# Optimization experiments

Hardware: AMD Instinct MI355X
Metric: run time of the kernel (lower is better)

Reference implementation:

```python
import jax, jax.numpy as jnp
import numpy as np

K = 2  # top-k slots from init kwargs


def setup_inputs() -> dict:
    key = jax.random.key(0)
    ks = jax.random.split(key, 6)
    B, T, d, E, dff = 2, 2048, 512, 8, 2048
    x = jax.random.normal(ks[0], (B, T, d), dtype=jnp.float32)
    Wg = jax.random.normal(ks[1], (d, E), dtype=jnp.float32) * 0.02
    W1 = jax.random.normal(ks[2], (E, d, dff), dtype=jnp.float32) * 0.02
    b1 = jnp.zeros((E, dff), dtype=jnp.float32)
    W2 = jax.random.normal(ks[3], (E, dff, d), dtype=jnp.float32) * 0.02
    b2 = jnp.zeros((E, d), dtype=jnp.float32)
    return {"x": x, "Wg": Wg, "W1": W1, "b1": b1, "W2": W2, "b2": b2}


def reference(x, Wg, W1, b1, W2, b2):
    # Gate: softmax over experts, top-k probs renormalized. Note: in the
    # original code the per-expert gather/scatter masks partition the tokens,
    # so dispatched_input == x * p_i (full weighted input), and ALL experts'
    # MLPs are applied to it and summed (tf.add_n). We reproduce that math.
    logits = jnp.einsum('btd,de->bte', x, Wg)          # [B,T,E]
    probs = jax.nn.softmax(logits, axis=-1)
    top_p, _top_i = jax.lax.top_k(probs, K)            # [B,T,K]
    top_p = top_p / jnp.sum(top_p, axis=-1, keepdims=True)
    b2_sum = jnp.sum(b2, axis=0)                        # sum of all experts' output biases
    out = jnp.zeros_like(x)
    for i in range(K):  # small fixed loop over top-k slots
        w_in = x * top_p[..., i:i + 1]                  # [B,T,d]
        # every expert runs on the full weighted input (faithful to source)
        h = jax.nn.gelu(
            jnp.einsum('btd,edf->ebtf', w_in, W1) + b1[:, None, None, :],
            approximate=False)                           # [E,B,T,dff]
        out = out + jnp.einsum('ebtf,efd->btd', h, W2) + b2_sum
    return out
```

## Files before the change

### kernel.cpp

```cpp
#include <hip/hip_runtime.h>
#include <hip/hip_bf16.h>
#include <cstdint>

#define TOKENS 4096
#define DMODEL 512
#define NEXP 8
#define DFF 2048

typedef short s16x8 __attribute__((ext_vector_type(8)));
typedef short s16x4 __attribute__((ext_vector_type(4)));
typedef float f32x4 __attribute__((ext_vector_type(4)));
typedef unsigned int u32x2 __attribute__((ext_vector_type(2)));

__device__ __forceinline__ float bf2f(short h) {
    unsigned int u = ((unsigned int)(unsigned short)h) << 16;
    return __uint_as_float(u);
}
__device__ __forceinline__ short f2bf(float f) {
    unsigned int u = __float_as_uint(f);
    u += 0x7fffu + ((u >> 16) & 1u);
    return (short)(u >> 16);
}
__device__ __forceinline__ unsigned int cvtpk_bf16(float a, float b) {
    unsigned int r;
    asm volatile("v_cvt_pk_bf16_f32 %0, %1, %2" : "=v"(r) : "v"(a), "v"(b));
    return r;
}
#define GP_C0 2.3022084f
#define GP_C1 0.10294330f
__device__ __forceinline__ float gelu_pair(float x0, float x1) {
    float z0 = x0 * fmaf(x0 * x0, GP_C1, GP_C0);
    float z1 = x1 * fmaf(x1 * x1, GP_C1, GP_C0);
    float e0 = __builtin_amdgcn_exp2f(z0);
    float e1 = __builtin_amdgcn_exp2f(z1);
    float t0 = 1.0f + e0, t1 = 1.0f + e1;
    float R = __builtin_amdgcn_rcpf(t0 * t1);
    float num = fmaf(x0, t1, x1 * t0);
    return fmaf(-num, R, x0 + x1);
}
__device__ __forceinline__ void gload_lds16(const void* g, void* l) {
    __builtin_amdgcn_global_load_lds((const __attribute__((address_space(1))) void*)g,
                                     (__attribute__((address_space(3))) void*)l, 16, 0, 0);
}

__global__ void gate_cvt_kernel(const float* __restrict__ x, const float* __restrict__ Wg,
                                float* __restrict__ s0, float* __restrict__ s1,
                                short* __restrict__ xb) {
    int wave = threadIdx.x >> 6;
    int lane = threadIdx.x & 63;
    int t = blockIdx.x * 4 + wave;
    const float* xr = x + (size_t)t * DMODEL + lane * 8;
    float4 xa = *(const float4*)(xr);
    float4 xv2 = *(const float4*)(xr + 4);
    float xv[8] = {xa.x, xa.y, xa.z, xa.w, xv2.x, xv2.y, xv2.z, xv2.w};
    s16x8 v;
#pragma unroll
    for (int j = 0; j < 8; j++) v[j] = f2bf(xv[j]);
    *(s16x8*)&xb[(size_t)t * DMODEL + lane * 8] = v;

    float lg[8];
#pragma unroll
    for (int e = 0; e < 8; e++) lg[e] = 0.f;
#pragma unroll
    for (int j = 0; j < 8; j++) {
        const float4* wr = (const float4*)(Wg + (size_t)(lane * 8 + j) * NEXP);
        float4 wa = wr[0], wb = wr[1];
        lg[0] = fmaf(xv[j], wa.x, lg[0]);
        lg[1] = fmaf(xv[j], wa.y, lg[1]);
        lg[2] = fmaf(xv[j], wa.z, lg[2]);
        lg[3] = fmaf(xv[j], wa.w, lg[3]);
        lg[4] = fmaf(xv[j], wb.x, lg[4]);
        lg[5] = fmaf(xv[j], wb.y, lg[5]);
        lg[6] = fmaf(xv[j], wb.z, lg[6]);
        lg[7] = fmaf(xv[j], wb.w, lg[7]);
    }
#pragma unroll
    for (int off = 32; off > 0; off >>= 1) {
#pragma unroll
        for (int e = 0; e < 8; e++) lg[e] += __shfl_xor(lg[e], off, 64);
    }
    float l0 = lg[0]; int i0 = 0;
#pragma unroll
    for (int e = 1; e < 8; e++) { if (lg[e] > l0) { l0 = lg[e]; i0 = e; } }
    float l1 = -3.4e38f;
#pragma unroll
    for (int e = 0; e < 8; e++) { if (e != i0 && lg[e] > l1) l1 = lg[e]; }
    float p1 = expf(l1 - l0);
    float sa = 1.0f / (1.0f + p1);
    if (lane == 0) { s0[t] = sa; s1[t] = p1 * sa; }
}

__global__ void transpose_cvt2_kernel(const float* __restrict__ W1, short* __restrict__ w1t,
                                      const float* __restrict__ W2, short* __restrict__ w2t) {
    __shared__ float t[64][33];
    int b = blockIdx.y;
    int bid = blockIdx.x;
    const float* ip;
    short* op;
    int R, C, tx, ty;
    if (bid < 512) {
        R = 512; C = 2048; tx = bid & 31; ty = bid >> 5;
        ip = W1 + (size_t)b * R * C; op = w1t + (size_t)b * R * C;
    } else {
        int id = bid - 512;
        R = 2048; C = 512; tx = id & 7; ty = id >> 3;
        ip = W2 + (size_t)b * R * C; op = w2t + (size_t)b * R * C;
    }
    int c0 = tx * 64, r0 = ty * 32;
    int tid = threadIdx.x;
    int lr = tid >> 3, lc8 = (tid & 7) * 8;
    const float* src = &ip[(size_t)(r0 + lr) * C + c0 + lc8];
    float4 v0 = *(const float4*)src;
    float4 v1 = *(const float4*)(src + 4);
    t[lc8 + 0][lr] = v0.x; t[lc8 + 1][lr] = v0.y; t[lc8 + 2][lr] = v0.z; t[lc8 + 3][lr] = v0.w;
    t[lc8 + 4][lr] = v1.x; t[lc8 + 5][lr] = v1.y; t[lc8 + 6][lr] = v1.z; t[lc8 + 7][lr] = v1.w;
    __syncthreads();
    int sc = tid >> 2, sk = (tid & 3) * 8;
    s16x8 o;
#pragma unroll
    for (int j = 0; j < 8; j++) o[j] = f2bf(t[sc][sk + j]);
    *(s16x8*)&op[(size_t)(c0 + sc) * R + r0 + sk] = o;
}

__launch_bounds__(256, 2)
__global__ void gemm1_kernel(const short* __restrict__ xb, const short* __restrict__ w1t,
                             const float* __restrict__ s0v, const float* __restrict__ s1v,
                             const float* __restrict__ b1, short* __restrict__ H) {
    __shared__ short Al[128 * 64];
    __shared__ short Bl[128 * 64];
    __shared__ float ls0[128], ls1[128], lb1[128];
    int d = blockIdx.x;
    int e = d & 7;
    int tno = d >> 3;
    int n0 = (tno & 15) * 128;
    int m0 = (tno >> 4) * 128;
    const short* A = xb;
    const short* B = w1t + (size_t)e * DFF * DMODEL;
    short* Ho = H + (size_t)e * TOKENS * DFF;

    int tid = threadIdx.x;
    int lane = tid & 63;
    int w = tid >> 6;
    int m_off = (w >> 1) * 64;
    int n_off = (w & 1) * 64;

    if (tid < 128) {
        ls0[tid] = s0v[m0 + tid];
        ls1[tid] = s1v[m0 + tid];
        lb1[tid] = b1[(size_t)e * DFF + n0 + tid];
    }

    int srow = lane >> 3;
    int schunk = (lane & 7) ^ srow;
    int q = lane >> 4;

    f32x4 acc[4][4];
#pragma unroll
    for (int mi = 0; mi < 4; mi++)
#pragma unroll
        for (int ni = 0; ni < 4; ni++) acc[mi][ni] = (f32x4){0.f, 0.f, 0.f, 0.f};

    for (int k0 = 0; k0 < DMODEL; k0 += 64) {
#pragma unroll
        for (int c = 0; c < 4; c++) {
            int seg = c * 4 + w;
            gload_lds16(&A[(size_t)(m0 + seg * 8 + srow) * DMODEL + k0 + schunk * 8],
                        &Al[seg * 512]);
            gload_lds16(&B[(size_t)(n0 + seg * 8 + srow) * DMODEL + k0 + schunk * 8],
                        &Bl[seg * 512]);
        }
        __syncthreads();
#pragma unroll
        for (int ks = 0; ks < 2; ks++) {
            s16x8 af[4], bfr[4];
#pragma unroll
            for (int mi = 0; mi < 4; mi++) {
                int r = m_off + mi * 16 + (lane & 15);
                int cp = (ks * 4 + q) ^ (r & 7);
                af[mi] = *(const s16x8*)&Al[r * 64 + cp * 8];
            }
#pragma unroll
            for (int ni = 0; ni < 4; ni++) {
                int r = n_off + ni * 16 + (lane & 15);
                int cp = (ks * 4 + q) ^ (r & 7);
                bfr[ni] = *(const s16x8*)&Bl[r * 64 + cp * 8];
            }
#pragma unroll
            for (int mi = 0; mi < 4; mi++)
#pragma unroll
                for (int ni = 0; ni < 4; ni++)
                    acc[mi][ni] = __builtin_amdgcn_mfma_f32_16x16x32_bf16(bfr[ni], af[mi], acc[mi][ni], 0, 0, 0);
        }
        __syncthreads();
    }
    {
        int mcol = lane & 15;
        int nrow4 = (lane >> 4) * 4;
#pragma unroll
        for (int mi = 0; mi < 4; mi++) {
            int m = m_off + mi * 16 + mcol;
            float sa = ls0[m], sb = ls1[m];
#pragma unroll
            for (int ni = 0; ni < 4; ni++) {
                int nb = n_off + ni * 16 + nrow4;
                float4 bb = *(const float4*)&lb1[nb];
                float bv[4] = {bb.x, bb.y, bb.z, bb.w};
                float h4[4];
#pragma unroll
                for (int r = 0; r < 4; r++) {
                    float a = acc[mi][ni][r];
                    h4[r] = gelu_pair(fmaf(sa, a, bv[r]), fmaf(sb, a, bv[r]));
                }
                u32x2 pv;
                pv[0] = cvtpk_bf16(h4[0], h4[1]);
                pv[1] = cvtpk_bf16(h4[2], h4[3]);
                *(u32x2*)&Ho[(size_t)(m0 + m) * DFF + n0 + nb] = pv;
            }
        }
    }
}

__launch_bounds__(256, 2)
__global__ void gemm2_kernel(const short* __restrict__ H, const short* __restrict__ w2t,
                             short* __restrict__ partb) {
    __shared__ short Al[128 * 64];
    __shared__ short Bl[128 * 64];
    int d = blockIdx.x;
    int e = d & 7;
    int tno = d >> 3;
    int n0 = (tno & 3) * 128;
    int m0 = (tno >> 2) * 128;
    const short* A = H + (size_t)e * TOKENS * DFF;
    const short* B = w2t + (size_t)e * DMODEL * DFF;
    short* Pe = partb + (size_t)e * TOKENS * DMODEL;

    int tid = threadIdx.x;
    int lane = tid & 63;
    int w = tid >> 6;
    int m_off = (w >> 1) * 64;
    int n_off = (w & 1) * 64;

    int srow = lane >> 3;
    int schunk = (lane & 7) ^ srow;
    int q = lane >> 4;

    f32x4 acc[4][4];
#pragma unroll
    for (int mi = 0; mi < 4; mi++)
#pragma unroll
        for (int ni = 0; ni < 4; ni++) acc[mi][ni] = (f32x4){0.f, 0.f, 0.f, 0.f};

    for (int k0 = 0; k0 < DFF; k0 += 64) {
#pragma unroll
        for (int c = 0; c < 4; c++) {
            int seg = c * 4 + w;
            gload_lds16(&A[(size_t)(m0 + seg * 8 + srow) * DFF + k0 + schunk * 8],
                        &Al[seg * 512]);
            gload_lds16(&B[(size_t)(n0 + seg * 8 + srow) * DFF + k0 + schunk * 8],
                        &Bl[seg * 512]);
        }
        __syncthreads();
#pragma unroll
        for (int ks = 0; ks < 2; ks++) {
            s16x8 af[4], bfr[4];
#pragma unroll
            for (int mi = 0; mi < 4; mi++) {
                int r = m_off + mi * 16 + (lane & 15);
                int cp = (ks * 4 + q) ^ (r & 7);
                af[mi] = *(const s16x8*)&Al[r * 64 + cp * 8];
            }
#pragma unroll
            for (int ni = 0; ni < 4; ni++) {
                int r = n_off + ni * 16 + (lane & 15);
                int cp = (ks * 4 + q) ^ (r & 7);
                bfr[ni] = *(const s16x8*)&Bl[r * 64 + cp * 8];
            }
#pragma unroll
            for (int mi = 0; mi < 4; mi++)
#pragma unroll
                for (int ni = 0; ni < 4; ni++)
                    acc[mi][ni] = __builtin_amdgcn_mfma_f32_16x16x32_bf16(bfr[ni], af[mi], acc[mi][ni], 0, 0, 0);
        }
        __syncthreads();
    }

    {
        int mcol = lane & 15;
        int nrow4 = (lane >> 4) * 4;
#pragma unroll
        for (int mi = 0; mi < 4; mi++) {
            int m = m0 + m_off + mi * 16 + mcol;
#pragma unroll
            for (int ni = 0; ni < 4; ni++) {
                int nb = n0 + n_off + ni * 16 + nrow4;
                u32x2 pv;
                pv[0] = cvtpk_bf16(acc[mi][ni][0], acc[mi][ni][1]);
                pv[1] = cvtpk_bf16(acc[mi][ni][2], acc[mi][ni][3]);
                *(u32x2*)&Pe[(size_t)m * DMODEL + nb] = pv;
            }
        }
    }
}

__global__ void reduce_kernel(const short* __restrict__ partb, const float* __restrict__ b2,
                              float* __restrict__ out) {
    int i = (blockIdx.x * 256 + threadIdx.x) * 8;
    if (i >= TOKENS * DMODEL) return;
    int n = i & (DMODEL - 1);
    float s[8] = {0.f, 0.f, 0.f, 0.f, 0.f, 0.f, 0.f, 0.f};
#pragma unroll
    for (int e = 0; e < 8; e++) {
        s16x8 p = *(const s16x8*)&partb[(size_t)e * TOKENS * DMODEL + i];
        float4 ba = *(const float4*)&b2[(size_t)e * DMODEL + n];
        float4 bb = *(const float4*)&b2[(size_t)e * DMODEL + n + 4];
        s[0] += bf2f(p[0]) + 2.f * ba.x;
        s[1] += bf2f(p[1]) + 2.f * ba.y;
        s[2] += bf2f(p[2]) + 2.f * ba.z;
        s[3] += bf2f(p[3]) + 2.f * ba.w;
        s[4] += bf2f(p[4]) + 2.f * bb.x;
        s[5] += bf2f(p[5]) + 2.f * bb.y;
        s[6] += bf2f(p[6]) + 2.f * bb.z;
        s[7] += bf2f(p[7]) + 2.f * bb.w;
    }
    float4 o0 = {s[0], s[1], s[2], s[3]};
    float4 o1 = {s[4], s[5], s[6], s[7]};
    *(float4*)&out[i] = o0;
    *(float4*)&out[i + 4] = o1;
}

extern "C" void kernel_launch(void* const* d_in, const int* in_sizes, int n_in,
                              void* d_out, int out_size, void* d_ws, size_t ws_size,
                              hipStream_t stream) {
    const float* x  = (const float*)d_in[0];
    const float* Wg = (const float*)d_in[1];
    const float* W1 = (const float*)d_in[2];
    const float* b1 = (const float*)d_in[3];
    const float* W2 = (const float*)d_in[4];
    const float* b2 = (const float*)d_in[5];
    float* out = (float*)d_out;

    char* ws = (char*)d_ws;
    float* s0  = (float*)(ws);
    float* s1  = (float*)(ws + 16384);
    short* xb  = (short*)(ws + 32768);
    short* w1t = (short*)(ws + 32768 + 4194304);
    short* w2t = (short*)(ws + 32768 + 4194304 + 16777216);
    short* Hb  = (short*)(ws + 32768 + 4194304 + 2ull * 16777216);
    short* partb = (short*)(ws + 32768 + 4194304 + 2ull * 16777216 + 134217728);

    hipLaunchKernelGGL(gate_cvt_kernel, dim3(1024), dim3(256), 0, stream, x, Wg, s0, s1, xb);
    hipLaunchKernelGGL(transpose_cvt2_kernel, dim3(1024, 8), dim3(256), 0, stream, W1, w1t, W2, w2t);
    hipLaunchKernelGGL(gemm1_kernel, dim3(4096), dim3(256), 0, stream, xb, w1t, s0, s1, b1, Hb);
    hipLaunchKernelGGL(gemm2_kernel, dim3(1024), dim3(256), 0, stream, Hb, w2t, partb);
    hipLaunchKernelGGL(reduce_kernel, dim3(1024), dim3(256), 0, stream, partb, b2, out);
}
```

Before: 206.2 us.

## Restructure gemm2 into 256x256 tiles with double-buffered LDS and phased MFMA

```diff
diff --git a/kernel.cpp b/kernel.cpp
--- a/kernel.cpp
+++ b/kernel.cpp
@@ -11,6 +11,8 @@
 typedef short s16x4 __attribute__((ext_vector_type(4)));
 typedef float f32x4 __attribute__((ext_vector_type(4)));
 typedef unsigned int u32x2 __attribute__((ext_vector_type(2)));
+
+#define MEMFENCE asm volatile("" ::: "memory")
 
 __device__ __forceinline__ float bf2f(short h) {
     unsigned int u = ((unsigned int)(unsigned short)h) << 16;
@@ -220,79 +222,176 @@
     }
 }
 
-__launch_bounds__(256, 2)
+__launch_bounds__(512, 1)
 __global__ void gemm2_kernel(const short* __restrict__ H, const short* __restrict__ w2t,
                              short* __restrict__ partb) {
-    __shared__ short Al[128 * 64];
-    __shared__ short Bl[128 * 64];
+    __shared__ short Al[2][256 * 64];
+    __shared__ short Bl[2][256 * 64];
     int d = blockIdx.x;
     int e = d & 7;
     int tno = d >> 3;
-    int n0 = (tno & 3) * 128;
-    int m0 = (tno >> 2) * 128;
-    const short* A = H + (size_t)e * TOKENS * DFF;
-    const short* B = w2t + (size_t)e * DMODEL * DFF;
+    int n0 = (tno & 1) * 256;
+    int m0 = (tno >> 1) * 256;
+    const short* A = H + (size_t)e * TOKENS * DFF + (size_t)m0 * DFF;
+    const short* B = w2t + (size_t)e * DMODEL * DFF + (size_t)n0 * DFF;
     short* Pe = partb + (size_t)e * TOKENS * DMODEL;
 
     int tid = threadIdx.x;
     int lane = tid & 63;
     int w = tid >> 6;
-    int m_off = (w >> 1) * 64;
-    int n_off = (w & 1) * 64;
+    int wr = w >> 2;
+    int wc = w & 3;
+    int q = lane >> 4;
+    int l15 = lane & 15;
 
     int srow = lane >> 3;
     int schunk = (lane & 7) ^ srow;
-    int q = lane >> 4;
-
-    f32x4 acc[4][4];
-#pragma unroll
-    for (int mi = 0; mi < 4; mi++)
+
+    f32x4 acc[8][4];
+#pragma unroll
+    for (int mi = 0; mi < 8; mi++)
 #pragma unroll
         for (int ni = 0; ni < 4; ni++) acc[mi][ni] = (f32x4){0.f, 0.f, 0.f, 0.f};
 
-    for (int k0 = 0; k0 < DFF; k0 += 64) {
-#pragma unroll
-        for (int c = 0; c < 4; c++) {
-            int seg = c * 4 + w;
-            gload_lds16(&A[(size_t)(m0 + seg * 8 + srow) * DFF + k0 + schunk * 8],
-                        &Al[seg * 512]);
-            gload_lds16(&B[(size_t)(n0 + seg * 8 + srow) * DFF + k0 + schunk * 8],
-                        &Bl[seg * 512]);
-        }
-        __syncthreads();
-#pragma unroll
-        for (int ks = 0; ks < 2; ks++) {
-            s16x8 af[4], bfr[4];
-#pragma unroll
-            for (int mi = 0; mi < 4; mi++) {
-                int r = m_off + mi * 16 + (lane & 15);
-                int cp = (ks * 4 + q) ^ (r & 7);
-                af[mi] = *(const s16x8*)&Al[r * 64 + cp * 8];
-            }
+    const int NT = DFF / 64;
+
+#define STAGE_HALF(SRC, DSTBUF, K0, HH)                                            \
+    {                                                                              \
+        _Pragma("unroll")                                                          \
+        for (int c = 0; c < 2; c++) {                                              \
+            int seg = (HH) * 16 + c * 8 + w;                                       \
+            gload_lds16(&SRC[(size_t)(seg * 8 + srow) * DFF + (K0) + schunk * 8],  \
+                        &DSTBUF[seg * 512]);                                       \
+        }                                                                          \
+    }
+
+    STAGE_HALF(A, (&Al[0][0]), 0, 0)
+    STAGE_HALF(A, (&Al[0][0]), 0, 1)
+    STAGE_HALF(B, (&Bl[0][0]), 0, 0)
+    STAGE_HALF(B, (&Bl[0][0]), 0, 1)
+
+    for (int t = 0; t < NT; t++) {
+        int db = t & 1;
+        const short* Ac = &Al[db][0];
+        const short* Bc = &Bl[db][0];
+        short* An = &Al[db ^ 1][0];
+        short* Bn = &Bl[db ^ 1][0];
+        int k1 = (t + 1) * 64;
+        bool more = (t + 1 < NT);
+
+        s16x8 af[4][2], bfA[2][2], bfB[2][2];
+
+        if (more) {
+            STAGE_HALF(A, An, k1, 0)
+            STAGE_HALF(B, Bn, k1, 0)
+            asm volatile("s_waitcnt vmcnt(4)" ::: "memory");
+        } else {
+            asm volatile("s_waitcnt vmcnt(0)" ::: "memory");
+        }
+        __builtin_amdgcn_s_barrier();
+        MEMFENCE;
+#pragma unroll
+        for (int mi = 0; mi < 4; mi++) {
+            int r = wr * 128 + mi * 16 + l15;
+#pragma unroll
+            for (int ks = 0; ks < 2; ks++) {
+                int cp = (ks * 4 + q) ^ (r & 7);
+                af[mi][ks] = *(const s16x8*)&Ac[r * 64 + cp * 8];
+            }
+        }
+#pragma unroll
+        for (int ni = 0; ni < 2; ni++) {
+            int r = wc * 64 + ni * 16 + l15;
+#pragma unroll
+            for (int ks = 0; ks < 2; ks++) {
+                int cp = (ks * 4 + q) ^ (r & 7);
+                bfA[ni][ks] = *(const s16x8*)&Bc[r * 64 + cp * 8];
+            }
+        }
+        __builtin_amdgcn_s_setprio(1);
+#pragma unroll
+        for (int ks = 0; ks < 2; ks++)
+#pragma unroll
+            for (int mi = 0; mi < 4; mi++)
+#pragma unroll
+                for (int ni = 0; ni < 2; ni++)
+                    acc[mi][ni] = __builtin_amdgcn_mfma_f32_16x16x32_bf16(bfA[ni][ks], af[mi][ks], acc[mi][ni], 0, 0, 0);
+        __builtin_amdgcn_s_setprio(0);
+        MEMFENCE;
+        __builtin_amdgcn_s_barrier();
+        MEMFENCE;
+
+        if (more) {
+            STAGE_HALF(A, An, k1, 1)
+            STAGE_HALF(B, Bn, k1, 1)
+        }
+#pragma unroll
+        for (int ni = 0; ni < 2; ni++) {
+            int r = wc * 64 + (ni + 2) * 16 + l15;
+#pragma unroll
+            for (int ks = 0; ks < 2; ks++) {
+                int cp = (ks * 4 + q) ^ (r & 7);
+                bfB[ni][ks] = *(const s16x8*)&Bc[r * 64 + cp * 8];
+            }
+        }
+        __builtin_amdgcn_s_setprio(1);
+#pragma unroll
+        for (int ks = 0; ks < 2; ks++)
+#pragma unroll
+            for (int mi = 0; mi < 4; mi++)
+#pragma unroll
+                for (int ni = 0; ni < 2; ni++)
+                    acc[mi][ni + 2] = __builtin_amdgcn_mfma_f32_16x16x32_bf16(bfB[ni][ks], af[mi][ks], acc[mi][ni + 2], 0, 0, 0);
+        __builtin_amdgcn_s_setprio(0);
+        MEMFENCE;
+        __builtin_amdgcn_s_barrier();
+        MEMFENCE;
+
+#pragma unroll
+        for (int mi = 0; mi < 4; mi++) {
+            int r = wr * 128 + (mi + 4) * 16 + l15;
+#pragma unroll
+            for (int ks = 0; ks < 2; ks++) {
+                int cp = (ks * 4 + q) ^ (r & 7);
+                af[mi][ks] = *(const s16x8*)&Ac[r * 64 + cp * 8];
+            }
+        }
+        __builtin_amdgcn_s_setprio(1);
+#pragma unroll
+        for (int ks = 0; ks < 2; ks++)
+#pragma unroll
+            for (int mi = 0; mi < 4; mi++)
+#pragma unroll
+                for (int ni = 0; ni < 2; ni++)
+                    acc[mi + 4][ni] = __builtin_amdgcn_mfma_f32_16x16x32_bf16(bfA[ni][ks], af[mi][ks], acc[mi + 4][ni], 0, 0, 0);
+        __builtin_amdgcn_s_setprio(0);
+        MEMFENCE;
+        __builtin_amdgcn_s_barrier();
+        MEMFENCE;
+
+        __builtin_amdgcn_s_setprio(1);
+#pragma unroll
+        for (int ks = 0; ks < 2; ks++)
+#pragma unroll
+            for (int mi = 0; mi < 4; mi++)
+#pragma unroll
+                for (int ni = 0; ni < 2; ni++)
+                    acc[mi + 4][ni + 2] = __builtin_amdgcn_mfma_f32_16x16x32_bf16(bfB[ni][ks], af[mi][ks], acc[mi + 4][ni + 2], 0, 0, 0);
+        __builtin_amdgcn_s_setprio(0);
+        MEMFENCE;
+        __builtin_amdgcn_s_barrier();
+        MEMFENCE;
+    }
+#undef STAGE_HALF
+
+    {
+        int nrow4 = (lane >> 4) * 4;
+#pragma unroll
+        for (int mi = 0; mi < 8; mi++) {
+            int m = m0 + wr * 128 + mi * 16 + l15;
 #pragma unroll
             for (int ni = 0; ni < 4; ni++) {
-                int r = n_off + ni * 16 + (lane & 15);
-                int cp = (ks * 4 + q) ^ (r & 7);
-                bfr[ni] = *(const s16x8*)&Bl[r * 64 + cp * 8];
-            }
-#pragma unroll
-            for (int mi = 0; mi < 4; mi++)
-#pragma unroll
-                for (int ni = 0; ni < 4; ni++)
-                    acc[mi][ni] = __builtin_amdgcn_mfma_f32_16x16x32_bf16(bfr[ni], af[mi], acc[mi][ni], 0, 0, 0);
-        }
-        __syncthreads();
-    }
-
-    {
-        int mcol = lane & 15;
-        int nrow4 = (lane >> 4) * 4;
-#pragma unroll
-        for (int mi = 0; mi < 4; mi++) {
-            int m = m0 + m_off + mi * 16 + mcol;
-#pragma unroll
-            for (int ni = 0; ni < 4; ni++) {
-                int nb = n0 + n_off + ni * 16 + nrow4;
+                int nb = n0 + wc * 64 + ni * 16 + nrow4;
                 u32x2 pv;
                 pv[0] = cvtpk_bf16(acc[mi][ni][0], acc[mi][ni][1]);
                 pv[1] = cvtpk_bf16(acc[mi][ni][2], acc[mi][ni][3]);
@@ -351,6 +450,6 @@
     hipLaunchKernelGGL(gate_cvt_kernel, dim3(1024), dim3(256), 0, stream, x, Wg, s0, s1, xb);
     hipLaunchKernelGGL(transpose_cvt2_kernel, dim3(1024, 8), dim3(256), 0, stream, W1, w1t, W2, w2t);
     hipLaunchKernelGGL(gemm1_kernel, dim3(4096), dim3(256), 0, stream, xb, w1t, s0, s1, b1, Hb);
-    hipLaunchKernelGGL(gemm2_kernel, dim3(1024), dim3(256), 0, stream, Hb, w2t, partb);
+    hipLaunchKernelGGL(gemm2_kernel, dim3(256), dim3(512), 0, stream, Hb, w2t, partb);
     hipLaunchKernelGGL(reduce_kernel, dim3(1024), dim3(256), 0, stream, partb, b2, out);
 }
```

Result: slower. 217.2 us (+5.3%).
